# Performance work log

Hardware: AMD Instinct MI355X
Metric: run time of the kernel (lower is better)

Reference implementation:

```python
import jax, jax.numpy as jnp
import numpy as np

N_NODES = 50000
N_RELATIONS = 8


def _rgcn_layer(x, src, dst, etype, W, root, bias):
    # PyG RGCNConv (aggr='mean'): out[n] = sum_r mean_{(s->n) in rel r} x[s] @ W[r] + x[n] @ root + bias
    N, d = x.shape
    R = W.shape[0]
    seg = etype * N + dst                                  # combined (relation, dst) segment id
    msg = x[src]                                           # [E, d] gather
    agg = jax.ops.segment_sum(msg, seg, num_segments=R * N)
    cnt = jax.ops.segment_sum(jnp.ones((src.shape[0],), x.dtype), seg, num_segments=R * N)
    agg = agg / jnp.maximum(cnt, 1.0)[:, None]             # mean aggregation (0 if no edges)
    agg = agg.reshape(R, N, d)
    return jnp.einsum('rnd,rdh->nh', agg, W) + x @ root + bias


def setup_inputs() -> dict:
    key = jax.random.key(0)
    ks = jax.random.split(key, 10)
    d_in, d_hid, d_out = 128, 128, 64
    E = 800000
    x = jax.random.normal(ks[0], (N_NODES, d_in), dtype=jnp.float32)
    edge_index = jax.random.randint(ks[1], (2, E), 0, N_NODES, dtype=jnp.int64)
    edge_type = jax.random.randint(ks[2], (E,), 0, N_RELATIONS, dtype=jnp.int64)
    s = 0.05
    W1 = jax.random.normal(ks[3], (N_RELATIONS, d_in, d_hid), dtype=jnp.float32) * s
    root1 = jax.random.normal(ks[4], (d_in, d_hid), dtype=jnp.float32) * s
    bias1 = jnp.zeros((d_hid,), dtype=jnp.float32)
    W2 = jax.random.normal(ks[5], (N_RELATIONS, d_hid, d_out), dtype=jnp.float32) * s
    root2 = jax.random.normal(ks[6], (d_hid, d_out), dtype=jnp.float32) * s
    bias2 = jnp.zeros((d_out,), dtype=jnp.float32)
    return {"x": x, "edge_index": edge_index, "edge_type": edge_type,
            "W1": W1, "root1": root1, "bias1": bias1,
            "W2": W2, "root2": root2, "bias2": bias2}


def reference(x, edge_index, edge_type, W1, root1, bias1, W2, root2, bias2):
    src, dst = edge_index[0], edge_index[1]
    h = _rgcn_layer(x, src, dst, edge_type, W1, root1, bias1)
    h = jax.nn.relu(h)
    out = _rgcn_layer(h, src, dst, edge_type, W2, root2, bias2)
    return out
```

## Files before the change

kernel.cpp:

```cpp
#include <hip/hip_runtime.h>
#include <hip/hip_bf16.h>


#define D_IN 128
#define NREL 8

typedef short bf16x8 __attribute__((ext_vector_type(8)));
typedef float f32x4 __attribute__((ext_vector_type(4)));

__device__ __forceinline__ ushort cvbf(float f) {
    unsigned u = __float_as_uint(f);
    return (ushort)((u + 0x7FFFu + ((u >> 16) & 1u)) >> 16);
}
__device__ __forceinline__ float bflo(unsigned v) { return __uint_as_float(v << 16); }
__device__ __forceinline__ float bfhi(unsigned v) { return __uint_as_float(v & 0xFFFF0000u); }

__global__ void to_bf16_kernel(const float* __restrict__ in,
                               ushort* __restrict__ out, int n4) {
    int i = blockIdx.x * blockDim.x + threadIdx.x;
    if (i >= n4) return;
    float4 v = ((const float4*)in)[i];
    ushort4 o;
    o.x = cvbf(v.x); o.y = cvbf(v.y); o.z = cvbf(v.z); o.w = cvbf(v.w);
    ((ushort4*)out)[i] = o;
}

__global__ void wt_transform_kernel(const float* __restrict__ W,
                                    const float* __restrict__ root,
                                    ushort* __restrict__ Wt, int NCOLS) {
    int i = blockIdx.x * blockDim.x + threadIdx.x;
    int tot = (NREL + 1) * D_IN * NCOLS;
    if (i >= tot) return;
    int s = i / (D_IN * NCOLS);
    int r = i - s * D_IN * NCOLS;
    int k = r / NCOLS;
    int n = r - k * NCOLS;
    float v = (s < NREL) ? W[(size_t)s * D_IN * NCOLS + (size_t)k * NCOLS + n]
                         : root[(size_t)k * NCOLS + n];
    int byteoff = (k << 1) ^ ((n & 7) << 4);
    Wt[(size_t)s * NCOLS * D_IN + (size_t)n * D_IN + (byteoff >> 1)] = cvbf(v);
}

__global__ void count_kernel(const int* __restrict__ dst,
                             const int* __restrict__ et,
                             int* __restrict__ cnt, int E, int N) {
    int e = blockIdx.x * blockDim.x + threadIdx.x;
    if (e < E) atomicAdd(&cnt[et[e] * N + dst[e]], 1);
}

__global__ void scan_block_sum(const int* __restrict__ cnt,
                               int* __restrict__ bsum, int nseg) {
    __shared__ int s[256];
    int base = blockIdx.x * 1024 + threadIdx.x * 4;
    int v = 0;
#pragma unroll
    for (int i = 0; i < 4; ++i) {
        int idx = base + i;
        if (idx < nseg) v += cnt[idx];
    }
    s[threadIdx.x] = v;
    __syncthreads();
    for (int off = 128; off > 0; off >>= 1) {
        if (threadIdx.x < off) s[threadIdx.x] += s[threadIdx.x + off];
        __syncthreads();
    }
    if (threadIdx.x == 0) bsum[blockIdx.x] = s[0];
}

__global__ void scan_bsum(int* __restrict__ bsum, int nb) {
    __shared__ int s[512];
    int t = threadIdx.x;
    int my = (t < nb) ? bsum[t] : 0;
    s[t] = my;
    __syncthreads();
    for (int off = 1; off < 512; off <<= 1) {
        int v = (t >= off) ? s[t - off] : 0;
        __syncthreads();
        s[t] += v;
        __syncthreads();
    }
    if (t < nb) bsum[t] = s[t] - my;
}

__global__ void scan_write(const int* __restrict__ cnt,
                           const int* __restrict__ bsum,
                           int* __restrict__ off, int nseg) {
    __shared__ int s[256];
    int t = threadIdx.x;
    int base = blockIdx.x * 1024 + t * 4;
    int v[4];
    int sum = 0;
#pragma unroll
    for (int i = 0; i < 4; ++i) {
        int idx = base + i;
        v[i] = (idx < nseg) ? cnt[idx] : 0;
        sum += v[i];
    }
    s[t] = sum;
    __syncthreads();
    int my = sum;
    for (int o = 1; o < 256; o <<= 1) {
        int x = (t >= o) ? s[t - o] : 0;
        __syncthreads();
        s[t] += x;
        __syncthreads();
    }
    int pre = s[t] - my + bsum[blockIdx.x];
#pragma unroll
    for (int i = 0; i < 4; ++i) {
        int idx = base + i;
        if (idx < nseg) {
            off[idx] = pre;
            pre += v[i];
        }
    }
}

__global__ void bucket_kernel(const int* __restrict__ src,
                              const int* __restrict__ dst,
                              const int* __restrict__ et,
                              int* __restrict__ off,
                              int* __restrict__ sids, int E, int N) {
    int e = blockIdx.x * blockDim.x + threadIdx.x;
    if (e < E) {
        int seg = et[e] * N + dst[e];
        int pos = atomicAdd(&off[seg], 1);
        sids[pos] = src[e];
    }
}

template <int NCOLS, bool RELU, bool OUTBF16>
__global__ __launch_bounds__(256) void fused_gemm_kernel(
    const ushort* __restrict__ feat,
    const int* __restrict__ sids,
    const int* __restrict__ endoff,
    const ushort* __restrict__ Wt,
    const float* __restrict__ bias,
    void* __restrict__ outp,
    int N) {
    constexpr int NT = NCOLS / 16;
    __shared__ ushort Bt[NCOLS * D_IN];

    const int tid = threadIdx.x;
    const int wave = tid >> 6;
    const int lane = tid & 63;
    const int c = lane & 15;
    const int g = lane >> 4;
    const int rb = blockIdx.x * 64 + wave * 16;
    const int arow = min(rb + c, N - 1);

    f32x4 acc[NT];
#pragma unroll
    for (int t = 0; t < NT; ++t) acc[t] = (f32x4){0.f, 0.f, 0.f, 0.f};

    for (int s = 0; s < NREL + 1; ++s) {
        {
            const uint4* srcw = (const uint4*)(Wt + (size_t)s * NCOLS * D_IN);
            uint4* dstw = (uint4*)Bt;
#pragma unroll
            for (int i = 0; i < (NCOLS * D_IN) / (8 * 256); ++i)
                dstw[tid + i * 256] = srcw[tid + i * 256];
        }
        __syncthreads();

        bf16x8 afr[4];
        if (s < NREL) {
            int seg = s * N + arow;
            int end = endoff[seg];
            int start = (seg == 0) ? 0 : endoff[seg - 1];
            int deg = end - start;
            float ac[4][8];
#pragma unroll
            for (int q = 0; q < 4; ++q)
#pragma unroll
                for (int j = 0; j < 8; ++j) ac[q][j] = 0.0f;
            for (int e = start; e < end; ++e) {
                int id = sids[e];
                const ushort* row = feat + (size_t)id * D_IN + 8 * g;
#pragma unroll
                for (int q = 0; q < 4; ++q) {
                    uint4 v = *(const uint4*)(row + 32 * q);
                    ac[q][0] += bflo(v.x); ac[q][1] += bfhi(v.x);
                    ac[q][2] += bflo(v.y); ac[q][3] += bfhi(v.y);
                    ac[q][4] += bflo(v.z); ac[q][5] += bfhi(v.z);
                    ac[q][6] += bflo(v.w); ac[q][7] += bfhi(v.w);
                }
            }
            float inv = (deg > 0) ? 1.0f / (float)deg : 0.0f;
#pragma unroll
            for (int q = 0; q < 4; ++q) {
                unsigned w0 = (unsigned)cvbf(ac[q][0] * inv) | ((unsigned)cvbf(ac[q][1] * inv) << 16);
                unsigned w1 = (unsigned)cvbf(ac[q][2] * inv) | ((unsigned)cvbf(ac[q][3] * inv) << 16);
                unsigned w2 = (unsigned)cvbf(ac[q][4] * inv) | ((unsigned)cvbf(ac[q][5] * inv) << 16);
                unsigned w3 = (unsigned)cvbf(ac[q][6] * inv) | ((unsigned)cvbf(ac[q][7] * inv) << 16);
                uint4 packed = make_uint4(w0, w1, w2, w3);
                afr[q] = *(bf16x8*)&packed;
            }
        } else {
            const ushort* row = feat + (size_t)arow * D_IN + 8 * g;
#pragma unroll
            for (int q = 0; q < 4; ++q) afr[q] = *(const bf16x8*)(row + 32 * q);
        }

#pragma unroll
        for (int q = 0; q < 4; ++q) {
            const int kt = q * 32;
#pragma unroll
            for (int t = 0; t < NT; ++t) {
                int n = t * 16 + c;
                int byteoff = n * 256 + ((kt * 2 + g * 16) ^ ((n & 7) << 4));
                bf16x8 b = *(const bf16x8*)((const char*)Bt + byteoff);
                acc[t] = __builtin_amdgcn_mfma_f32_16x16x32_bf16(afr[q], b, acc[t], 0, 0, 0);
            }
        }
        __syncthreads();
    }

#pragma unroll
    for (int t = 0; t < NT; ++t) {
        float bv = bias[t * 16 + c];
#pragma unroll
        for (int r = 0; r < 4; ++r) {
            int orow = rb + 4 * g + r;
            if (orow < N) {
                float v = acc[t][r] + bv;
                if (RELU) v = fmaxf(v, 0.0f);
                if (OUTBF16)
                    ((ushort*)outp)[(size_t)orow * NCOLS + t * 16 + c] = cvbf(v);
                else
                    ((float*)outp)[(size_t)orow * NCOLS + t * 16 + c] = v;
            }
        }
    }
}

extern "C" void kernel_launch(void* const* d_in, const int* in_sizes, int n_in,
                              void* d_out, int out_size, void* d_ws, size_t ws_size,
                              hipStream_t stream) {
    const float* x = (const float*)d_in[0];
    const int* ei = (const int*)d_in[1];
    const int* et = (const int*)d_in[2];
    const float* W1 = (const float*)d_in[3];
    const float* root1 = (const float*)d_in[4];
    const float* bias1 = (const float*)d_in[5];
    const float* W2 = (const float*)d_in[6];
    const float* root2 = (const float*)d_in[7];
    const float* bias2 = (const float*)d_in[8];
    float* out = (float*)d_out;

    const int N = in_sizes[0] / D_IN;
    const int E = in_sizes[2];
    const int* src = ei;
    const int* dst = ei + E;
    const int NSEG = NREL * N;
    const int NB = (NSEG + 1023) / 1024;

    ushort* xb = (ushort*)d_ws;
    ushort* hb = xb + (size_t)N * D_IN;
    ushort* wt1 = hb + (size_t)N * D_IN;
    ushort* wt2 = wt1 + (size_t)(NREL + 1) * D_IN * D_IN;
    int* off = (int*)(wt2 + (size_t)(NREL + 1) * 64 * D_IN);
    int* sids = off + NSEG;
    int* cnt = sids + E;
    int* bsum = cnt + NSEG;

    to_bf16_kernel<<<(N * D_IN / 4 + 255) / 256, 256, 0, stream>>>(x, xb, N * D_IN / 4);
    wt_transform_kernel<<<((NREL + 1) * D_IN * 128 + 255) / 256, 256, 0, stream>>>(
        W1, root1, wt1, 128);
    wt_transform_kernel<<<((NREL + 1) * D_IN * 64 + 255) / 256, 256, 0, stream>>>(
        W2, root2, wt2, 64);

    hipMemsetAsync(cnt, 0, (size_t)NSEG * sizeof(int), stream);
    count_kernel<<<(E + 255) / 256, 256, 0, stream>>>(dst, et, cnt, E, N);
    scan_block_sum<<<NB, 256, 0, stream>>>(cnt, bsum, NSEG);
    scan_bsum<<<1, 512, 0, stream>>>(bsum, NB);
    scan_write<<<NB, 256, 0, stream>>>(cnt, bsum, off, NSEG);
    bucket_kernel<<<(E + 255) / 256, 256, 0, stream>>>(src, dst, et, off, sids, E, N);

    const int gemmBlocks = (N + 63) / 64;

    fused_gemm_kernel<128, true, true><<<gemmBlocks, 256, 0, stream>>>(
        xb, sids, off, wt1, bias1, hb, N);

    fused_gemm_kernel<64, false, false><<<gemmBlocks, 256, 0, stream>>>(
        hb, sids, off, wt2, bias2, out, N);
}
```

Baseline: 258.8 us.

## Double-buffer weight staging, prefetch next relation aggregate, and node-major segment layout

Weight tiles now sit in two shared-memory buffers. The next relation's weights are staged and its neighbor aggregation built while the MFMAs for the current relation run, which overlaps the gather latency with compute and drops one barrier per relation. Segment ids change from relation-major to node-major, so each node's eight relation offsets are contiguous and are loaded once at kernel start. The XOR swizzle is replaced by a padded row stride of 136. Shared-memory use doubles and register pressure rises from the extra A fragments and offsets, which may lower occupancy.

```diff
diff --git a/kernel.cpp b/kernel.cpp
--- a/kernel.cpp
+++ b/kernel.cpp
@@ -4,6 +4,7 @@
 
 #define D_IN 128
 #define NREL 8
+#define BTSTRIDE 136
 
 typedef short bf16x8 __attribute__((ext_vector_type(8)));
 typedef float f32x4 __attribute__((ext_vector_type(4)));
@@ -37,15 +38,14 @@
     int n = r - k * NCOLS;
     float v = (s < NREL) ? W[(size_t)s * D_IN * NCOLS + (size_t)k * NCOLS + n]
                          : root[(size_t)k * NCOLS + n];
-    int byteoff = (k << 1) ^ ((n & 7) << 4);
-    Wt[(size_t)s * NCOLS * D_IN + (size_t)n * D_IN + (byteoff >> 1)] = cvbf(v);
+    Wt[((size_t)s * NCOLS + n) * BTSTRIDE + k] = cvbf(v);
 }
 
 __global__ void count_kernel(const int* __restrict__ dst,
                              const int* __restrict__ et,
                              int* __restrict__ cnt, int E, int N) {
     int e = blockIdx.x * blockDim.x + threadIdx.x;
-    if (e < E) atomicAdd(&cnt[et[e] * N + dst[e]], 1);
+    if (e < E) atomicAdd(&cnt[dst[e] * NREL + et[e]], 1);
 }
 
 __global__ void scan_block_sum(const int* __restrict__ cnt,
@@ -123,7 +123,7 @@
                               int* __restrict__ sids, int E, int N) {
     int e = blockIdx.x * blockDim.x + threadIdx.x;
     if (e < E) {
-        int seg = et[e] * N + dst[e];
+        int seg = dst[e] * NREL + et[e];
         int pos = atomicAdd(&off[seg], 1);
         sids[pos] = src[e];
     }
@@ -139,7 +139,8 @@
     void* __restrict__ outp,
     int N) {
     constexpr int NT = NCOLS / 16;
-    __shared__ ushort Bt[NCOLS * D_IN];
+    constexpr int SEGW = NCOLS * BTSTRIDE / 8;
+    __shared__ __align__(16) ushort Bt[2][NCOLS * BTSTRIDE];
 
     const int tid = threadIdx.x;
     const int wave = tid >> 6;
@@ -149,71 +150,89 @@
     const int rb = blockIdx.x * 64 + wave * 16;
     const int arow = min(rb + c, N - 1);
 
+    int so[9];
+    {
+        int b = arow * NREL;
+        so[0] = (b == 0) ? 0 : endoff[b - 1];
+#pragma unroll
+        for (int s = 1; s <= NREL; ++s) so[s] = endoff[b + s - 1];
+    }
+
     f32x4 acc[NT];
 #pragma unroll
     for (int t = 0; t < NT; ++t) acc[t] = (f32x4){0.f, 0.f, 0.f, 0.f};
 
+    const ushort* myrow = feat + (size_t)arow * D_IN + 8 * g;
+
+    bf16x8 aC[4], aN[4];
+#define BUILD_A(S, DST)                                                        \
+    do {                                                                       \
+        if ((S) < NREL) {                                                      \
+            int start = so[(S)], end = so[(S) + 1];                            \
+            int deg = end - start;                                             \
+            float ac[4][8];                                                    \
+            _Pragma("unroll") for (int q = 0; q < 4; ++q)                      \
+                _Pragma("unroll") for (int j = 0; j < 8; ++j) ac[q][j] = 0.f;  \
+            for (int e = start; e < end; ++e) {                                \
+                int id = sids[e];                                              \
+                const ushort* row = feat + (size_t)id * D_IN + 8 * g;          \
+                _Pragma("unroll") for (int q = 0; q < 4; ++q) {                \
+                    uint4 v = *(const uint4*)(row + 32 * q);                   \
+                    ac[q][0] += bflo(v.x); ac[q][1] += bfhi(v.x);              \
+                    ac[q][2] += bflo(v.y); ac[q][3] += bfhi(v.y);              \
+                    ac[q][4] += bflo(v.z); ac[q][5] += bfhi(v.z);              \
+                    ac[q][6] += bflo(v.w); ac[q][7] += bfhi(v.w);              \
+                }                                                              \
+            }                                                                  \
+            float inv = (deg > 0) ? 1.0f / (float)deg : 0.0f;                  \
+            _Pragma("unroll") for (int q = 0; q < 4; ++q) {                    \
+                uint4 pk;                                                      \
+                pk.x = (unsigned)cvbf(ac[q][0] * inv) |                        \
+                       ((unsigned)cvbf(ac[q][1] * inv) << 16);                 \
+                pk.y = (unsigned)cvbf(ac[q][2] * inv) |                        \
+                       ((unsigned)cvbf(ac[q][3] * inv) << 16);                 \
+                pk.z = (unsigned)cvbf(ac[q][4] * inv) |                        \
+                       ((unsigned)cvbf(ac[q][5] * inv) << 16);                 \
+                pk.w = (unsigned)cvbf(ac[q][6] * inv) |                        \
+                       ((unsigned)cvbf(ac[q][7] * inv) << 16);                 \
+                DST[q] = *(bf16x8*)&pk;                                        \
+            }                                                                  \
+        } else {                                                               \
+            _Pragma("unroll") for (int q = 0; q < 4; ++q)                      \
+                DST[q] = *(const bf16x8*)(myrow + 32 * q);                     \
+        }                                                                      \
+    } while (0)
+
+#define STAGE(S, BUF)                                                          \
+    do {                                                                       \
+        const uint4* srcw = (const uint4*)(Wt + (size_t)(S)*NCOLS * BTSTRIDE); \
+        uint4* dstw = (uint4*)(Bt[(BUF)]);                                     \
+        for (int i = tid; i < SEGW; i += 256) dstw[i] = srcw[i];               \
+    } while (0)
+
+    STAGE(0, 0);
+    BUILD_A(0, aC);
+    __syncthreads();
+
     for (int s = 0; s < NREL + 1; ++s) {
-        {
-            const uint4* srcw = (const uint4*)(Wt + (size_t)s * NCOLS * D_IN);
-            uint4* dstw = (uint4*)Bt;
-#pragma unroll
-            for (int i = 0; i < (NCOLS * D_IN) / (8 * 256); ++i)
-                dstw[tid + i * 256] = srcw[tid + i * 256];
+        const int cb = s & 1;
+        if (s < NREL) {
+            STAGE(s + 1, cb ^ 1);
+            BUILD_A(s + 1, aN);
         }
-        __syncthreads();
-
-        bf16x8 afr[4];
-        if (s < NREL) {
-            int seg = s * N + arow;
-            int end = endoff[seg];
-            int start = (seg == 0) ? 0 : endoff[seg - 1];
-            int deg = end - start;
-            float ac[4][8];
-#pragma unroll
-            for (int q = 0; q < 4; ++q)
-#pragma unroll
-                for (int j = 0; j < 8; ++j) ac[q][j] = 0.0f;
-            for (int e = start; e < end; ++e) {
-                int id = sids[e];
-                const ushort* row = feat + (size_t)id * D_IN + 8 * g;
-#pragma unroll
-                for (int q = 0; q < 4; ++q) {
-                    uint4 v = *(const uint4*)(row + 32 * q);
-                    ac[q][0] += bflo(v.x); ac[q][1] += bfhi(v.x);
-                    ac[q][2] += bflo(v.y); ac[q][3] += bfhi(v.y);
-                    ac[q][4] += bflo(v.z); ac[q][5] += bfhi(v.z);
-                    ac[q][6] += bflo(v.w); ac[q][7] += bfhi(v.w);
-                }
-            }
-            float inv = (deg > 0) ? 1.0f / (float)deg : 0.0f;
-#pragma unroll
-            for (int q = 0; q < 4; ++q) {
-                unsigned w0 = (unsigned)cvbf(ac[q][0] * inv) | ((unsigned)cvbf(ac[q][1] * inv) << 16);
-                unsigned w1 = (unsigned)cvbf(ac[q][2] * inv) | ((unsigned)cvbf(ac[q][3] * inv) << 16);
-                unsigned w2 = (unsigned)cvbf(ac[q][4] * inv) | ((unsigned)cvbf(ac[q][5] * inv) << 16);
-                unsigned w3 = (unsigned)cvbf(ac[q][6] * inv) | ((unsigned)cvbf(ac[q][7] * inv) << 16);
-                uint4 packed = make_uint4(w0, w1, w2, w3);
-                afr[q] = *(bf16x8*)&packed;
-            }
-        } else {
-            const ushort* row = feat + (size_t)arow * D_IN + 8 * g;
-#pragma unroll
-            for (int q = 0; q < 4; ++q) afr[q] = *(const bf16x8*)(row + 32 * q);
-        }
-
+        const ushort* bt = Bt[cb];
 #pragma unroll
         for (int q = 0; q < 4; ++q) {
-            const int kt = q * 32;
 #pragma unroll
             for (int t = 0; t < NT; ++t) {
-                int n = t * 16 + c;
-                int byteoff = n * 256 + ((kt * 2 + g * 16) ^ ((n & 7) << 4));
-                bf16x8 b = *(const bf16x8*)((const char*)Bt + byteoff);
-                acc[t] = __builtin_amdgcn_mfma_f32_16x16x32_bf16(afr[q], b, acc[t], 0, 0, 0);
+                const ushort* bp = bt + (t * 16 + c) * BTSTRIDE + q * 32 + 8 * g;
+                bf16x8 b = *(const bf16x8*)bp;
+                acc[t] = __builtin_amdgcn_mfma_f32_16x16x32_bf16(aC[q], b, acc[t], 0, 0, 0);
             }
         }
         __syncthreads();
+#pragma unroll
+        for (int q = 0; q < 4; ++q) aC[q] = aN[q];
     }
 
 #pragma unroll
@@ -232,6 +251,8 @@
             }
         }
     }
+#undef BUILD_A
+#undef STAGE
 }
 
 extern "C" void kernel_launch(void* const* d_in, const int* in_sizes, int n_in,
@@ -258,8 +279,8 @@
     ushort* xb = (ushort*)d_ws;
     ushort* hb = xb + (size_t)N * D_IN;
     ushort* wt1 = hb + (size_t)N * D_IN;
-    ushort* wt2 = wt1 + (size_t)(NREL + 1) * D_IN * D_IN;
-    int* off = (int*)(wt2 + (size_t)(NREL + 1) * 64 * D_IN);
+    ushort* wt2 = wt1 + (size_t)(NREL + 1) * D_IN * BTSTRIDE;
+    int* off = (int*)(wt2 + (size_t)(NREL + 1) * 64 * BTSTRIDE);
     int* sids = off + NSEG;
     int* cnt = sids + E;
     int* bsum = cnt + NSEG;
```

Measured after the change: 314.2 us. +21.4%, slower.

## Reorder segments dst-major, drop LDS weight staging, split output columns across grid

Applied to the files above, without the earlier changes.

Segments are now indexed dst-major (dst*NREL+etype), so each row's eight relation ranges are contiguous and all nine offsets load up front. The GEMM no longer stages weights in shared memory with swizzling. It reads unswizzled bf16 weight fragments straight from global memory and computes the transposed MFMA product, letting each lane store four contiguous output columns. Output columns are split into 64-wide tiles over blockIdx.y, which gives layer 1 twice as many blocks. The cost is that the neighbour gather and mean in layer 1 are repeated for each column tile.

```diff
diff --git a/kernel.cpp b/kernel.cpp
--- a/kernel.cpp
+++ b/kernel.cpp
@@ -37,15 +37,14 @@
     int n = r - k * NCOLS;
     float v = (s < NREL) ? W[(size_t)s * D_IN * NCOLS + (size_t)k * NCOLS + n]
                          : root[(size_t)k * NCOLS + n];
-    int byteoff = (k << 1) ^ ((n & 7) << 4);
-    Wt[(size_t)s * NCOLS * D_IN + (size_t)n * D_IN + (byteoff >> 1)] = cvbf(v);
+    Wt[((size_t)s * NCOLS + n) * D_IN + k] = cvbf(v);
 }
 
 __global__ void count_kernel(const int* __restrict__ dst,
                              const int* __restrict__ et,
                              int* __restrict__ cnt, int E, int N) {
     int e = blockIdx.x * blockDim.x + threadIdx.x;
-    if (e < E) atomicAdd(&cnt[et[e] * N + dst[e]], 1);
+    if (e < E) atomicAdd(&cnt[dst[e] * NREL + et[e]], 1);
 }
 
 __global__ void scan_block_sum(const int* __restrict__ cnt,
@@ -123,13 +122,13 @@
                               int* __restrict__ sids, int E, int N) {
     int e = blockIdx.x * blockDim.x + threadIdx.x;
     if (e < E) {
-        int seg = et[e] * N + dst[e];
+        int seg = dst[e] * NREL + et[e];
         int pos = atomicAdd(&off[seg], 1);
         sids[pos] = src[e];
     }
 }
 
-template <int NCOLS, bool RELU, bool OUTBF16>
+template <bool RELU, bool OUTBF16>
 __global__ __launch_bounds__(256) void fused_gemm_kernel(
     const ushort* __restrict__ feat,
     const int* __restrict__ sids,
@@ -137,98 +136,105 @@
     const ushort* __restrict__ Wt,
     const float* __restrict__ bias,
     void* __restrict__ outp,
-    int N) {
-    constexpr int NT = NCOLS / 16;
-    __shared__ ushort Bt[NCOLS * D_IN];
-
+    int N, int NCOLS) {
     const int tid = threadIdx.x;
     const int wave = tid >> 6;
     const int lane = tid & 63;
     const int c = lane & 15;
     const int g = lane >> 4;
-    const int rb = blockIdx.x * 64 + wave * 16;
-    const int arow = min(rb + c, N - 1);
-
-    f32x4 acc[NT];
-#pragma unroll
-    for (int t = 0; t < NT; ++t) acc[t] = (f32x4){0.f, 0.f, 0.f, 0.f};
-
-    for (int s = 0; s < NREL + 1; ++s) {
-        {
-            const uint4* srcw = (const uint4*)(Wt + (size_t)s * NCOLS * D_IN);
-            uint4* dstw = (uint4*)Bt;
-#pragma unroll
-            for (int i = 0; i < (NCOLS * D_IN) / (8 * 256); ++i)
-                dstw[tid + i * 256] = srcw[tid + i * 256];
-        }
-        __syncthreads();
-
-        bf16x8 afr[4];
-        if (s < NREL) {
-            int seg = s * N + arow;
-            int end = endoff[seg];
-            int start = (seg == 0) ? 0 : endoff[seg - 1];
-            int deg = end - start;
-            float ac[4][8];
-#pragma unroll
-            for (int q = 0; q < 4; ++q)
-#pragma unroll
-                for (int j = 0; j < 8; ++j) ac[q][j] = 0.0f;
-            for (int e = start; e < end; ++e) {
-                int id = sids[e];
-                const ushort* row = feat + (size_t)id * D_IN + 8 * g;
-#pragma unroll
-                for (int q = 0; q < 4; ++q) {
-                    uint4 v = *(const uint4*)(row + 32 * q);
-                    ac[q][0] += bflo(v.x); ac[q][1] += bfhi(v.x);
-                    ac[q][2] += bflo(v.y); ac[q][3] += bfhi(v.y);
-                    ac[q][4] += bflo(v.z); ac[q][5] += bfhi(v.z);
-                    ac[q][6] += bflo(v.w); ac[q][7] += bfhi(v.w);
-                }
-            }
-            float inv = (deg > 0) ? 1.0f / (float)deg : 0.0f;
+    const int row = blockIdx.x * 64 + wave * 16 + c;
+    const int arow = min(row, N - 1);
+    const int colbase = blockIdx.y * 64;
+
+    int so[9];
+    {
+        int b = arow * NREL;
+        so[0] = (b == 0) ? 0 : endoff[b - 1];
+#pragma unroll
+        for (int s = 1; s <= NREL; ++s) so[s] = endoff[b + s - 1];
+    }
+
+    f32x4 acc[4];
+#pragma unroll
+    for (int t = 0; t < 4; ++t) acc[t] = (f32x4){0.f, 0.f, 0.f, 0.f};
+
+    const ushort* myrow = feat + (size_t)arow * D_IN + 8 * g;
+
+    {
+        bf16x8 bfrag[4];
+#pragma unroll
+        for (int q = 0; q < 4; ++q) bfrag[q] = *(const bf16x8*)(myrow + 32 * q);
+        const ushort* wseg = Wt + ((size_t)NREL * NCOLS + colbase) * D_IN;
+#pragma unroll
+        for (int q = 0; q < 4; ++q)
+#pragma unroll
+            for (int t = 0; t < 4; ++t) {
+                bf16x8 w = *(const bf16x8*)(wseg + (size_t)(t * 16 + c) * D_IN + q * 32 + 8 * g);
+                acc[t] = __builtin_amdgcn_mfma_f32_16x16x32_bf16(w, bfrag[q], acc[t], 0, 0, 0);
+            }
+    }
+
+    for (int s = 0; s < NREL; ++s) {
+        int start = so[s], end = so[s + 1];
+        int deg = end - start;
+        float ac[4][8];
+#pragma unroll
+        for (int q = 0; q < 4; ++q)
+#pragma unroll
+            for (int j = 0; j < 8; ++j) ac[q][j] = 0.f;
+        for (int e = start; e < end; ++e) {
+            int id = sids[e];
+            const ushort* fr = feat + (size_t)id * D_IN + 8 * g;
 #pragma unroll
             for (int q = 0; q < 4; ++q) {
-                unsigned w0 = (unsigned)cvbf(ac[q][0] * inv) | ((unsigned)cvbf(ac[q][1] * inv) << 16);
-                unsigned w1 = (unsigned)cvbf(ac[q][2] * inv) | ((unsigned)cvbf(ac[q][3] * inv) << 16);
-                unsigned w2 = (unsigned)cvbf(ac[q][4] * inv) | ((unsigned)cvbf(ac[q][5] * inv) << 16);
-                unsigned w3 = (unsigned)cvbf(ac[q][6] * inv) | ((unsigned)cvbf(ac[q][7] * inv) << 16);
-                uint4 packed = make_uint4(w0, w1, w2, w3);
-                afr[q] = *(bf16x8*)&packed;
-            }
-        } else {
-            const ushort* row = feat + (size_t)arow * D_IN + 8 * g;
-#pragma unroll
-            for (int q = 0; q < 4; ++q) afr[q] = *(const bf16x8*)(row + 32 * q);
-        }
-
+                uint4 v = *(const uint4*)(fr + 32 * q);
+                ac[q][0] += bflo(v.x); ac[q][1] += bfhi(v.x);
+                ac[q][2] += bflo(v.y); ac[q][3] += bfhi(v.y);
+                ac[q][4] += bflo(v.z); ac[q][5] += bfhi(v.z);
+                ac[q][6] += bflo(v.w); ac[q][7] += bfhi(v.w);
+            }
+        }
+        float inv = (deg > 0) ? 1.0f / (float)deg : 0.0f;
+        bf16x8 bfrag[4];
 #pragma unroll
         for (int q = 0; q < 4; ++q) {
-            const int kt = q * 32;
-#pragma unroll
-            for (int t = 0; t < NT; ++t) {
-                int n = t * 16 + c;
-                int byteoff = n * 256 + ((kt * 2 + g * 16) ^ ((n & 7) << 4));
-                bf16x8 b = *(const bf16x8*)((const char*)Bt + byteoff);
-                acc[t] = __builtin_amdgcn_mfma_f32_16x16x32_bf16(afr[q], b, acc[t], 0, 0, 0);
-            }
-        }
-        __syncthreads();
-    }
-
-#pragma unroll
-    for (int t = 0; t < NT; ++t) {
-        float bv = bias[t * 16 + c];
-#pragma unroll
-        for (int r = 0; r < 4; ++r) {
-            int orow = rb + 4 * g + r;
-            if (orow < N) {
-                float v = acc[t][r] + bv;
-                if (RELU) v = fmaxf(v, 0.0f);
-                if (OUTBF16)
-                    ((ushort*)outp)[(size_t)orow * NCOLS + t * 16 + c] = cvbf(v);
-                else
-                    ((float*)outp)[(size_t)orow * NCOLS + t * 16 + c] = v;
+            uint4 pk;
+            pk.x = (unsigned)cvbf(ac[q][0] * inv) | ((unsigned)cvbf(ac[q][1] * inv) << 16);
+            pk.y = (unsigned)cvbf(ac[q][2] * inv) | ((unsigned)cvbf(ac[q][3] * inv) << 16);
+            pk.z = (unsigned)cvbf(ac[q][4] * inv) | ((unsigned)cvbf(ac[q][5] * inv) << 16);
+            pk.w = (unsigned)cvbf(ac[q][6] * inv) | ((unsigned)cvbf(ac[q][7] * inv) << 16);
+            bfrag[q] = *(bf16x8*)&pk;
+        }
+        const ushort* wseg = Wt + ((size_t)s * NCOLS + colbase) * D_IN;
+#pragma unroll
+        for (int q = 0; q < 4; ++q)
+#pragma unroll
+            for (int t = 0; t < 4; ++t) {
+                bf16x8 w = *(const bf16x8*)(wseg + (size_t)(t * 16 + c) * D_IN + q * 32 + 8 * g);
+                acc[t] = __builtin_amdgcn_mfma_f32_16x16x32_bf16(w, bfrag[q], acc[t], 0, 0, 0);
+            }
+    }
+
+    if (row < N) {
+#pragma unroll
+        for (int t = 0; t < 4; ++t) {
+            int colb = colbase + t * 16 + 4 * g;
+            float4 bv = *(const float4*)(bias + colb);
+            float v0 = acc[t][0] + bv.x;
+            float v1 = acc[t][1] + bv.y;
+            float v2 = acc[t][2] + bv.z;
+            float v3 = acc[t][3] + bv.w;
+            if (RELU) {
+                v0 = fmaxf(v0, 0.f); v1 = fmaxf(v1, 0.f);
+                v2 = fmaxf(v2, 0.f); v3 = fmaxf(v3, 0.f);
+            }
+            if (OUTBF16) {
+                ushort4 o;
+                o.x = cvbf(v0); o.y = cvbf(v1); o.z = cvbf(v2); o.w = cvbf(v3);
+                *(ushort4*)((ushort*)outp + (size_t)row * NCOLS + colb) = o;
+            } else {
+                *(float4*)((float*)outp + (size_t)row * NCOLS + colb) =
+                    make_float4(v0, v1, v2, v3);
             }
         }
     }
@@ -277,11 +283,11 @@
     scan_write<<<NB, 256, 0, stream>>>(cnt, bsum, off, NSEG);
     bucket_kernel<<<(E + 255) / 256, 256, 0, stream>>>(src, dst, et, off, sids, E, N);
 
-    const int gemmBlocks = (N + 63) / 64;
-
-    fused_gemm_kernel<128, true, true><<<gemmBlocks, 256, 0, stream>>>(
-        xb, sids, off, wt1, bias1, hb, N);
-
-    fused_gemm_kernel<64, false, false><<<gemmBlocks, 256, 0, stream>>>(
-        hb, sids, off, wt2, bias2, out, N);
-}
+    const int rowBlocks = (N + 63) / 64;
+
+    fused_gemm_kernel<true, true><<<dim3(rowBlocks, 2), 256, 0, stream>>>(
+        xb, sids, off, wt1, bias1, hb, N, 128);
+
+    fused_gemm_kernel<false, false><<<dim3(rowBlocks, 1), 256, 0, stream>>>(
+        hb, sids, off, wt2, bias2, out, N, 64);
+}
```

Result: slower. 423.8 us (+63.8%).

## Use node-major CSR with 16-bit source ids and stage aggregated rows in LDS

Applied to the files above, without the earlier changes.

Segments are now keyed as dst*NREL+rel instead of rel*N+dst, so a node's nine offsets are contiguous and can be loaded once up front. Source ids are stored as 16-bit values, which halves index traffic. Each node's aggregation is now done by four threads, each reading 64 contiguous bytes. The mean row is written into a swizzled LDS A-tile, and the MFMA fragments are read back from there. The 16-bit ids only work while the node count stays below 65536, and the extra LDS tile raises shared-memory use per block.

```diff
diff --git a/kernel.cpp b/kernel.cpp
--- a/kernel.cpp
+++ b/kernel.cpp
@@ -45,7 +45,7 @@
                              const int* __restrict__ et,
                              int* __restrict__ cnt, int E, int N) {
     int e = blockIdx.x * blockDim.x + threadIdx.x;
-    if (e < E) atomicAdd(&cnt[et[e] * N + dst[e]], 1);
+    if (e < E) atomicAdd(&cnt[dst[e] * NREL + et[e]], 1);
 }
 
 __global__ void scan_block_sum(const int* __restrict__ cnt,
@@ -120,40 +120,59 @@
                               const int* __restrict__ dst,
                               const int* __restrict__ et,
                               int* __restrict__ off,
-                              int* __restrict__ sids, int E, int N) {
+                              ushort* __restrict__ sids, int E, int N) {
     int e = blockIdx.x * blockDim.x + threadIdx.x;
     if (e < E) {
-        int seg = et[e] * N + dst[e];
+        int seg = dst[e] * NREL + et[e];
         int pos = atomicAdd(&off[seg], 1);
-        sids[pos] = src[e];
+        sids[pos] = (ushort)src[e];
     }
 }
 
 template <int NCOLS, bool RELU, bool OUTBF16>
 __global__ __launch_bounds__(256) void fused_gemm_kernel(
     const ushort* __restrict__ feat,
-    const int* __restrict__ sids,
+    const ushort* __restrict__ sids,
     const int* __restrict__ endoff,
     const ushort* __restrict__ Wt,
     const float* __restrict__ bias,
     void* __restrict__ outp,
     int N) {
     constexpr int NT = NCOLS / 16;
-    __shared__ ushort Bt[NCOLS * D_IN];
+    __shared__ __align__(16) ushort At[64 * D_IN];
+    __shared__ __align__(16) ushort Bt[NCOLS * D_IN];
 
     const int tid = threadIdx.x;
     const int wave = tid >> 6;
     const int lane = tid & 63;
     const int c = lane & 15;
     const int g = lane >> 4;
-    const int rb = blockIdx.x * 64 + wave * 16;
-    const int arow = min(rb + c, N - 1);
+    const int rb = blockIdx.x * 64;
+    const int rbw = rb + wave * 16;
+
+    const int grp = tid >> 2;
+    const int gl = tid & 3;
+    const int anode = min(rb + grp, N - 1);
+
+    int so[NREL + 1];
+    {
+        int b = anode * NREL;
+        so[0] = (b == 0) ? 0 : endoff[b - 1];
+#pragma unroll
+        for (int i = 1; i <= NREL; ++i) so[i] = endoff[b + i - 1];
+    }
 
     f32x4 acc[NT];
 #pragma unroll
     for (int t = 0; t < NT; ++t) acc[t] = (f32x4){0.f, 0.f, 0.f, 0.f};
 
-    for (int s = 0; s < NREL + 1; ++s) {
+    const int mrow = wave * 16 + c;
+    const int mswz = (mrow & 7) << 4;
+    const int aswz = (grp & 7) << 4;
+    char* const arow_w = (char*)At + grp * 256;
+    const char* const arow_r = (const char*)At + mrow * 256;
+
+    for (int s = 0; s <= NREL; ++s) {
         {
             const uint4* srcw = (const uint4*)(Wt + (size_t)s * NCOLS * D_IN);
             uint4* dstw = (uint4*)Bt;
@@ -161,56 +180,62 @@
             for (int i = 0; i < (NCOLS * D_IN) / (8 * 256); ++i)
                 dstw[tid + i * 256] = srcw[tid + i * 256];
         }
-        __syncthreads();
-
-        bf16x8 afr[4];
-        if (s < NREL) {
-            int seg = s * N + arow;
-            int end = endoff[seg];
-            int start = (seg == 0) ? 0 : endoff[seg - 1];
-            int deg = end - start;
-            float ac[4][8];
-#pragma unroll
-            for (int q = 0; q < 4; ++q)
-#pragma unroll
-                for (int j = 0; j < 8; ++j) ac[q][j] = 0.0f;
-            for (int e = start; e < end; ++e) {
-                int id = sids[e];
-                const ushort* row = feat + (size_t)id * D_IN + 8 * g;
-#pragma unroll
-                for (int q = 0; q < 4; ++q) {
-                    uint4 v = *(const uint4*)(row + 32 * q);
-                    ac[q][0] += bflo(v.x); ac[q][1] += bfhi(v.x);
-                    ac[q][2] += bflo(v.y); ac[q][3] += bfhi(v.y);
-                    ac[q][4] += bflo(v.z); ac[q][5] += bfhi(v.z);
-                    ac[q][6] += bflo(v.w); ac[q][7] += bfhi(v.w);
-                }
+        {
+            float a[32];
+#pragma unroll
+            for (int j = 0; j < 32; ++j) a[j] = 0.f;
+            int st, en, deg;
+            if (s < NREL) { st = so[s]; en = so[s + 1]; deg = en - st; }
+            else { st = 0; en = 1; deg = 1; }
+            for (int e = st; e < en; ++e) {
+                int id = (s < NREL) ? (int)sids[e] : anode;
+                const ushort* row = feat + (size_t)id * D_IN + gl * 32;
+                uint4 v0 = *(const uint4*)(row);
+                uint4 v1 = *(const uint4*)(row + 8);
+                uint4 v2 = *(const uint4*)(row + 16);
+                uint4 v3 = *(const uint4*)(row + 24);
+                a[0] += bflo(v0.x);  a[1] += bfhi(v0.x);
+                a[2] += bflo(v0.y);  a[3] += bfhi(v0.y);
+                a[4] += bflo(v0.z);  a[5] += bfhi(v0.z);
+                a[6] += bflo(v0.w);  a[7] += bfhi(v0.w);
+                a[8] += bflo(v1.x);  a[9] += bfhi(v1.x);
+                a[10] += bflo(v1.y); a[11] += bfhi(v1.y);
+                a[12] += bflo(v1.z); a[13] += bfhi(v1.z);
+                a[14] += bflo(v1.w); a[15] += bfhi(v1.w);
+                a[16] += bflo(v2.x); a[17] += bfhi(v2.x);
+                a[18] += bflo(v2.y); a[19] += bfhi(v2.y);
+                a[20] += bflo(v2.z); a[21] += bfhi(v2.z);
+                a[22] += bflo(v2.w); a[23] += bfhi(v2.w);
+                a[24] += bflo(v3.x); a[25] += bfhi(v3.x);
+                a[26] += bflo(v3.y); a[27] += bfhi(v3.y);
+                a[28] += bflo(v3.z); a[29] += bfhi(v3.z);
+                a[30] += bflo(v3.w); a[31] += bfhi(v3.w);
             }
             float inv = (deg > 0) ? 1.0f / (float)deg : 0.0f;
 #pragma unroll
-            for (int q = 0; q < 4; ++q) {
-                unsigned w0 = (unsigned)cvbf(ac[q][0] * inv) | ((unsigned)cvbf(ac[q][1] * inv) << 16);
-                unsigned w1 = (unsigned)cvbf(ac[q][2] * inv) | ((unsigned)cvbf(ac[q][3] * inv) << 16);
-                unsigned w2 = (unsigned)cvbf(ac[q][4] * inv) | ((unsigned)cvbf(ac[q][5] * inv) << 16);
-                unsigned w3 = (unsigned)cvbf(ac[q][6] * inv) | ((unsigned)cvbf(ac[q][7] * inv) << 16);
-                uint4 packed = make_uint4(w0, w1, w2, w3);
-                afr[q] = *(bf16x8*)&packed;
+            for (int q2 = 0; q2 < 4; ++q2) {
+                uint4 pk;
+                pk.x = (unsigned)cvbf(a[q2 * 8 + 0] * inv) |
+                       ((unsigned)cvbf(a[q2 * 8 + 1] * inv) << 16);
+                pk.y = (unsigned)cvbf(a[q2 * 8 + 2] * inv) |
+                       ((unsigned)cvbf(a[q2 * 8 + 3] * inv) << 16);
+                pk.z = (unsigned)cvbf(a[q2 * 8 + 4] * inv) |
+                       ((unsigned)cvbf(a[q2 * 8 + 5] * inv) << 16);
+                pk.w = (unsigned)cvbf(a[q2 * 8 + 6] * inv) |
+                       ((unsigned)cvbf(a[q2 * 8 + 7] * inv) << 16);
+                *(uint4*)(arow_w + ((gl * 64 + q2 * 16) ^ aswz)) = pk;
             }
-        } else {
-            const ushort* row = feat + (size_t)arow * D_IN + 8 * g;
-#pragma unroll
-            for (int q = 0; q < 4; ++q) afr[q] = *(const bf16x8*)(row + 32 * q);
-        }
-
+        }
+        __syncthreads();
 #pragma unroll
         for (int q = 0; q < 4; ++q) {
-            const int kt = q * 32;
+            bf16x8 afr = *(const bf16x8*)(arow_r + ((q * 64 + g * 16) ^ mswz));
 #pragma unroll
             for (int t = 0; t < NT; ++t) {
                 int n = t * 16 + c;
-                int byteoff = n * 256 + ((kt * 2 + g * 16) ^ ((n & 7) << 4));
+                int byteoff = n * 256 + ((q * 64 + g * 16) ^ ((n & 7) << 4));
                 bf16x8 b = *(const bf16x8*)((const char*)Bt + byteoff);
-                acc[t] = __builtin_amdgcn_mfma_f32_16x16x32_bf16(afr[q], b, acc[t], 0, 0, 0);
+                acc[t] = __builtin_amdgcn_mfma_f32_16x16x32_bf16(afr, b, acc[t], 0, 0, 0);
             }
         }
         __syncthreads();
@@ -221,7 +246,7 @@
         float bv = bias[t * 16 + c];
 #pragma unroll
         for (int r = 0; r < 4; ++r) {
-            int orow = rb + 4 * g + r;
+            int orow = rbw + 4 * g + r;
             if (orow < N) {
                 float v = acc[t][r] + bv;
                 if (RELU) v = fmaxf(v, 0.0f);
@@ -259,9 +284,9 @@
     ushort* hb = xb + (size_t)N * D_IN;
     ushort* wt1 = hb + (size_t)N * D_IN;
     ushort* wt2 = wt1 + (size_t)(NREL + 1) * D_IN * D_IN;
-    int* off = (int*)(wt2 + (size_t)(NREL + 1) * 64 * D_IN);
-    int* sids = off + NSEG;
-    int* cnt = sids + E;
+    ushort* sids = wt2 + (size_t)(NREL + 1) * 64 * D_IN;
+    int* off = (int*)(sids + E);
+    int* cnt = off + NSEG;
     int* bsum = cnt + NSEG;
 
     to_bf16_kernel<<<(N * D_IN / 4 + 255) / 256, 256, 0, stream>>>(x, xb, N * D_IN / 4);
```

After: 273.8 us. 5.8% more time.
